# Performance work log

Measured on AMD Instinct MI355X. Metric: run time of the kernel, lower is better.

Reference implementation:

```python
import jax, jax.numpy as jnp
import numpy as np
import math

D_MODEL = 1024
NHEAD = 16
SEQ_LEN = 4096
K_PROJ = 16
HEAD_DIM = D_MODEL // NHEAD


def setup_inputs() -> dict:
    key = jax.random.key(0)
    ks = jax.random.split(key, 11)
    x = jax.random.normal(ks[0], (4, SEQ_LEN, D_MODEL), dtype=jnp.float32)
    s = 1.0 / math.sqrt(D_MODEL)
    Wq = jax.random.uniform(ks[1], (D_MODEL, D_MODEL), minval=-s, maxval=s)
    bq = jax.random.uniform(ks[2], (D_MODEL,), minval=-s, maxval=s)
    Wk = jax.random.uniform(ks[3], (D_MODEL, D_MODEL), minval=-s, maxval=s)
    bk = jax.random.uniform(ks[4], (D_MODEL,), minval=-s, maxval=s)
    Wv = jax.random.uniform(ks[5], (D_MODEL, D_MODEL), minval=-s, maxval=s)
    bv = jax.random.uniform(ks[6], (D_MODEL,), minval=-s, maxval=s)
    Wo = jax.random.uniform(ks[7], (D_MODEL, D_MODEL), minval=-s, maxval=s)
    bo = jax.random.uniform(ks[8], (D_MODEL,), minval=-s, maxval=s)
    E = jax.random.normal(ks[9], (NHEAD, K_PROJ, SEQ_LEN)) * 0.02
    F = jax.random.normal(ks[10], (NHEAD, K_PROJ, SEQ_LEN)) * 0.02
    return {"x": x, "Wq": Wq, "bq": bq, "Wk": Wk, "bk": bk,
            "Wv": Wv, "bv": bv, "Wo": Wo, "bo": bo, "E": E, "F": F}


def reference(x, Wq, bq, Wk, bk, Wv, bv, Wo, bo, E, F):
    B, N, D = x.shape
    # torch Linear: y = x @ W.T + b
    q = x @ Wq.T + bq
    k = x @ Wk.T + bk
    v = x @ Wv.T + bv
    # [B, H, N, Dh]
    def split_heads(t):
        return t.reshape(B, N, NHEAD, HEAD_DIM).transpose(0, 2, 1, 3)
    q, k, v = split_heads(q), split_heads(k), split_heads(v)
    # low-rank projections of K, V along sequence: [B, H, Kp, Dh]
    k_lin = jnp.einsum('bhnd,hkn->bhkd', k, E)
    v_lin = jnp.einsum('bhnd,hkn->bhkd', v, F)
    scores = jnp.einsum('bhnd,bhkd->bhnk', q, k_lin) / math.sqrt(HEAD_DIM)
    attn = jax.nn.softmax(scores, axis=-1)  # dropout is identity in eval
    out = jnp.einsum('bhnk,bhkd->bhnd', attn, v_lin)
    out = out.transpose(0, 2, 1, 3).reshape(B, N, D)
    return out @ Wo.T + bo
```

## Files before the change

kernel.cpp:

```cpp
#include <hip/hip_runtime.h>
#include <hip/hip_bf16.h>

#define SEQLEN 4096

typedef __bf16 bf16x8 __attribute__((ext_vector_type(8)));
typedef float f32x4 __attribute__((ext_vector_type(4)));
typedef __attribute__((ext_vector_type(8))) unsigned short u16x8;

__device__ inline float bf2f(unsigned short s) {
  union { unsigned u; float f; } t; t.u = ((unsigned)s) << 16; return t.f;
}
__device__ inline unsigned short f2bf(float f) {
  __hip_bfloat16 h = __float2bfloat16(f);
  return *reinterpret_cast<unsigned short*>(&h);
}

__device__ inline void gload_lds16(const void* g, void* l) {
  __builtin_amdgcn_global_load_lds(
      (const __attribute__((address_space(1))) unsigned int*)g,
      (__attribute__((address_space(3))) unsigned int*)l, 16, 0, 0);
}

__global__ void cvt_all(const float* __restrict__ x, const float* __restrict__ Wq,
                        const float* __restrict__ Wk, const float* __restrict__ Wv,
                        const float* __restrict__ Wo,
                        const float* __restrict__ bq, const float* __restrict__ bk,
                        const float* __restrict__ bv,
                        unsigned short* __restrict__ Xb,
                        unsigned short* __restrict__ Wqkv,
                        unsigned short* __restrict__ WoB, float* __restrict__ Bqkv) {
  long i = (long)blockIdx.x * 256 + threadIdx.x;
  const float* src;
  unsigned short* dst;
  long rel;
  if (i < 4194304) {
    src = x; dst = Xb; rel = i;
  } else if (i < 4456448) {
    src = Wq; dst = Wqkv; rel = i - 4194304;
  } else if (i < 4718592) {
    src = Wk; dst = Wqkv + 1048576; rel = i - 4456448;
  } else if (i < 4980736) {
    src = Wv; dst = Wqkv + 2097152; rel = i - 4718592;
  } else if (i < 5242880) {
    src = Wo; dst = WoB; rel = i - 4980736;
  } else if (i < 5243648) {
    long j = i - 5242880;
    const float* bsrc = (j < 256) ? bq : (j < 512) ? bk : bv;
    long jr = j & 255;
    reinterpret_cast<float4*>(Bqkv)[j] =
        reinterpret_cast<const float4*>(bsrc)[jr];
    return;
  } else {
    return;
  }
  float4 v = reinterpret_cast<const float4*>(src)[rel];
  ushort4 o;
  o.x = f2bf(v.x); o.y = f2bf(v.y); o.z = f2bf(v.z); o.w = f2bf(v.w);
  reinterpret_cast<ushort4*>(dst)[rel] = o;
}


#define MFMAQ(mh, nh, AR, BR)                                                   \
  __builtin_amdgcn_s_setprio(1);                                                \
  _Pragma("unroll")                                                             \
  for (int ks = 0; ks < 2; ++ks)                                                \
    _Pragma("unroll")                                                           \
    for (int mi = 0; mi < 4; ++mi)                                              \
      _Pragma("unroll")                                                         \
      for (int ni = 0; ni < 2; ++ni)                                            \
        acc[(mh) * 4 + mi][(nh) * 2 + ni] =                                     \
            __builtin_amdgcn_mfma_f32_16x16x32_bf16(                            \
                AR[mi][ks], BR[ni][ks], acc[(mh) * 4 + mi][(nh) * 2 + ni], 0, 0, 0); \
  __builtin_amdgcn_s_setprio(0);

#define LDA8(mi, sg) (*reinterpret_cast<const bf16x8*>(&as[((wr << 7) + (mi) * 16 + r16) * 64 + (sg) * 8]))
#define LDB8N(nh, ni, sg) (*reinterpret_cast<const bf16x8*>(&bs[(((nh) << 7) + (wc << 5) + (ni) * 16 + r16) * 64 + (sg) * 8]))

template <typename OUT_T>
__global__ __launch_bounds__(512, 2) void gemm8p(
    const unsigned short* __restrict__ A, const unsigned short* __restrict__ B,
    const float* __restrict__ bias, OUT_T* __restrict__ C, int M, int N, int K,
    int ldc) {
  extern __shared__ __align__(16) unsigned short lds[];

  const int tid = threadIdx.x;
  const int lane = tid & 63, wv = tid >> 6;
  const int wr = wv >> 2, wc = wv & 3;
  const int r16 = lane & 15, kg = lane >> 4;
  const int sg0 = (0 * 4 + kg) ^ (r16 & 7);
  const int sg1 = (1 * 4 + kg) ^ (r16 & 7);

  const int xcd = (int)blockIdx.x & 7;
  const int pos = (int)blockIdx.x >> 3;
  const int rpx = (M >> 8) >> 3;
  const int tile_m = xcd * rpx + (pos % rpx);
  const int tile_n = pos / rpx;
  const int brow = tile_m << 8, bcol = tile_n << 8;

  const unsigned short* Ag = A + (size_t)brow * K;
  const unsigned short* Bg = B + (size_t)bcol * K;

  const int sr = tid >> 3;
  const int sc = tid & 7;
  const int sgl = sc ^ (sr & 7);

  auto STG = [&](const unsigned short* G, unsigned short* dstbuf, int row0, int kt) {
    gload_lds16(G + (size_t)(row0 + sr) * K + (size_t)kt * 64 + sgl * 8,
                dstbuf + (row0 + sr) * 64 + sc * 8);
  };
  auto STGH = [&](int hw, int pb, int kt) {
    unsigned short* ab = lds + (pb << 14);
    unsigned short* bb = lds + 32768 + (pb << 14);
    if (hw == 0)      { STG(Ag, ab, 0, kt);   STG(Ag, ab, 128, kt); }
    else if (hw == 1) { STG(Bg, bb, 0, kt);   STG(Bg, bb, 64, kt); }
    else if (hw == 2) { STG(Bg, bb, 128, kt); STG(Bg, bb, 192, kt); }
    else              { STG(Ag, ab, 64, kt);  STG(Ag, ab, 192, kt); }
  };

  f32x4 acc[8][4];
#pragma unroll
  for (int m = 0; m < 8; ++m)
#pragma unroll
    for (int n = 0; n < 4; ++n) acc[m][n] = (f32x4)0.0f;

  const int NT = K >> 6;
  STGH(0, 0, 0); STGH(1, 0, 0); STGH(2, 0, 0); STGH(3, 0, 0);
  STGH(0, 1, 1); STGH(1, 1, 1); STGH(2, 1, 1);
  asm volatile("s_waitcnt vmcnt(6)" ::: "memory");
  __builtin_amdgcn_s_barrier();

  for (int t = 0; t < NT; ++t) {
    const int cur = t & 1;
    const unsigned short* as = lds + (cur << 14);
    const unsigned short* bs = lds + 32768 + (cur << 14);
    const int w1 = (t + 1 < NT) ? t + 1 : 0;
    const int w2 = (t + 2 < NT) ? t + 2 : t + 2 - NT;
    const int b1n = (t + 1) & 1;

    bf16x8 a[4][2], b0[2][2], b1[2][2];

    {
#pragma unroll
      for (int mi = 0; mi < 4; ++mi) { a[mi][0] = LDA8(mi, sg0); a[mi][1] = LDA8(mi, sg1); }
#pragma unroll
      for (int ni = 0; ni < 2; ++ni) { b0[ni][0] = LDB8N(0, ni, sg0); b0[ni][1] = LDB8N(0, ni, sg1); }
      STGH(3, b1n, w1);
      asm volatile("s_waitcnt lgkmcnt(8)" ::: "memory");
      __builtin_amdgcn_s_barrier();
      asm volatile("s_waitcnt lgkmcnt(0)" ::: "memory");
      MFMAQ(0, 0, a, b0);
      __builtin_amdgcn_s_barrier();
    }
    {
#pragma unroll
      for (int ni = 0; ni < 2; ++ni) { b1[ni][0] = LDB8N(1, ni, sg0); b1[ni][1] = LDB8N(1, ni, sg1); }
      STGH(0, cur, w2);
      __builtin_amdgcn_s_barrier();
      asm volatile("s_waitcnt lgkmcnt(0)" ::: "memory");
      MFMAQ(0, 1, a, b1);
      __builtin_amdgcn_s_barrier();
    }
    {
#pragma unroll
      for (int mi = 0; mi < 4; ++mi) { a[mi][0] = LDA8(4 + mi, sg0); a[mi][1] = LDA8(4 + mi, sg1); }
      STGH(1, cur, w2);
      __builtin_amdgcn_s_barrier();
      asm volatile("s_waitcnt lgkmcnt(0)" ::: "memory");
      MFMAQ(1, 1, a, b1);
      __builtin_amdgcn_s_barrier();
    }
    {
      STGH(2, cur, w2);
      MFMAQ(1, 0, a, b0);
      asm volatile("s_waitcnt vmcnt(6)" ::: "memory");
      __builtin_amdgcn_s_barrier();
    }
  }
  asm volatile("s_waitcnt vmcnt(0)" ::: "memory");

  if constexpr (sizeof(OUT_T) == 2) {
    __builtin_amdgcn_s_barrier();
    unsigned short* C2 = reinterpret_cast<unsigned short*>(C);
    float bvs[4];
#pragma unroll
    for (int n = 0; n < 4; ++n)
      bvs[n] = bias ? bias[bcol + ((n >> 1) << 7) + (wc << 5) + ((n & 1) << 4) + r16]
                    : 0.0f;
#pragma unroll
    for (int m = 0; m < 8; ++m) {
#pragma unroll
      for (int r = 0; r < 4; ++r) {
        int rw = m * 16 + kg * 4 + r;
        int xo = (rw & 12) << 2;
#pragma unroll
        for (int n = 0; n < 4; ++n) {
          lds[wv * 8192 + rw * 64 + ((n * 16 + r16) ^ xo)] =
              f2bf(acc[m][n][r] + bvs[n]);
        }
      }
    }
    __syncthreads();
#pragma unroll
    for (int p = 0; p < 16; ++p) {
      int grow = p * 16 + (tid >> 5);
      int g = tid & 31;
      int wvs = ((grow >> 7) << 2) + ((g >> 2) & 3);
      int row_l = grow & 127;
      int c4g = ((g >> 4) << 5) + ((g & 3) << 3);
      int src = wvs * 8192 + row_l * 64 + (c4g ^ ((row_l & 12) << 2));
      u16x8 vv = *reinterpret_cast<const u16x8*>(&lds[src]);
      *reinterpret_cast<u16x8*>(&C2[(size_t)(brow + grow) * ldc + bcol + g * 8]) = vv;
    }
  } else {
#pragma unroll
    for (int n = 0; n < 4; ++n) {
      int col = bcol + ((n >> 1) << 7) + (wc << 5) + ((n & 1) << 4) + r16;
      float bv = bias ? bias[col] : 0.0f;
#pragma unroll
      for (int m = 0; m < 8; ++m) {
#pragma unroll
        for (int r = 0; r < 4; ++r) {
          int row = brow + wr * 128 + m * 16 + kg * 4 + r;
          C[(size_t)row * ldc + col] = acc[m][n][r] + bv;
        }
      }
    }
  }
}

__global__ void kvlin_part(const unsigned short* __restrict__ qkv,
                           const float* __restrict__ E, const float* __restrict__ F,
                           float* __restrict__ part) {
  __shared__ __align__(16) unsigned short Ks[128 * 64], Vs[128 * 64];
  __shared__ __align__(16) float Es[16 * 128], Fs[16 * 128];
  const int tid = threadIdx.x;
  const int bid = blockIdx.x;
  const int bh = bid >> 3, ns = bid & 7;
  const int b = bh >> 4, h = bh & 15;
  const int d = tid & 63, kk = tid >> 6;
  float aK[4] = {0, 0, 0, 0}, aV[4] = {0, 0, 0, 0};
  for (int c = 0; c < 4; ++c) {
    int n0 = ns * 512 + c * 128;
#pragma unroll
    for (int it = 0; it < 4; ++it) {
      int f = it * 256 + tid;
      int row = f >> 3, ch = f & 7;
      const unsigned short* gk =
          qkv + (size_t)(b * SEQLEN + n0 + row) * 3072 + 1024 + h * 64 + ch * 8;
      gload_lds16(gk, &Ks[f * 8]);
      gload_lds16(gk + 1024, &Vs[f * 8]);
    }
#pragma unroll
    for (int it = 0; it < 2; ++it) {
      int f = it * 256 + tid;
      int k = f >> 5, ch = f & 31;
      const float* ge = E + (size_t)(h * 16 + k) * SEQLEN + n0 + ch * 4;
      const float* gf = F + (size_t)(h * 16 + k) * SEQLEN + n0 + ch * 4;
      gload_lds16(ge, &Es[f * 4]);
      gload_lds16(gf, &Fs[f * 4]);
    }
    __syncthreads();
    for (int n = 0; n < 128; ++n) {
      float kv = bf2f(Ks[n * 64 + d]);
      float vv = bf2f(Vs[n * 64 + d]);
#pragma unroll
      for (int j = 0; j < 4; ++j) {
        aK[j] += Es[(kk * 4 + j) * 128 + n] * kv;
        aV[j] += Fs[(kk * 4 + j) * 128 + n] * vv;
      }
    }
    __syncthreads();
  }
  size_t base = ((size_t)ns * 64 + bh) * 2048;
#pragma unroll
  for (int j = 0; j < 4; ++j) {
    part[base + (kk * 4 + j) * 64 + d] = aK[j];
    part[base + 1024 + (kk * 4 + j) * 64 + d] = aV[j];
  }
}

__global__ void kvlin_reduce(const float* __restrict__ part, float* __restrict__ out) {
  int i = blockIdx.x * 256 + threadIdx.x;
  float s = 0;
#pragma unroll
  for (int ns = 0; ns < 8; ++ns) s += part[(size_t)ns * 131072 + i];
  out[i] = s;
}

__global__ void attn_kernel(const unsigned short* __restrict__ qkv,
                            const float* __restrict__ kvlin,
                            unsigned short* __restrict__ aout) {
  __shared__ float kl[1024], vl[1024];
  const int tid = threadIdx.x;
  const int bid = blockIdx.x;
  const int bh = bid >> 4, nt = bid & 15;
  const int b = bh >> 4, h = bh & 15;
  for (int i = tid; i < 1024; i += 256) {
    kl[i] = kvlin[(size_t)bh * 2048 + i];
    vl[i] = kvlin[(size_t)bh * 2048 + 1024 + i];
  }
  __syncthreads();
  const int n = nt * 256 + tid;
  const unsigned short* qp = qkv + (size_t)(b * SEQLEN + n) * 3072 + h * 64;
  float q[64];
#pragma unroll
  for (int c2 = 0; c2 < 8; ++c2) {
    u16x8 v = *reinterpret_cast<const u16x8*>(qp + c2 * 8);
#pragma unroll
    for (int j = 0; j < 8; ++j) q[c2 * 8 + j] = bf2f(v[j]);
  }
  float s[16];
#pragma unroll
  for (int k = 0; k < 16; ++k) {
    float a = 0;
#pragma unroll
    for (int dd = 0; dd < 64; ++dd) a += q[dd] * kl[k * 64 + dd];
    s[k] = a * 0.125f;
  }
  float mx = s[0];
#pragma unroll
  for (int k = 1; k < 16; ++k) mx = fmaxf(mx, s[k]);
  float sum = 0;
#pragma unroll
  for (int k = 0; k < 16; ++k) { s[k] = __expf(s[k] - mx); sum += s[k]; }
  float inv = 1.0f / sum;
#pragma unroll
  for (int k = 0; k < 16; ++k) s[k] *= inv;
  unsigned short* op = aout + (size_t)(b * SEQLEN + n) * 1024 + h * 64;
#pragma unroll
  for (int d0 = 0; d0 < 8; ++d0) {
    float o[8] = {0, 0, 0, 0, 0, 0, 0, 0};
#pragma unroll
    for (int k = 0; k < 16; ++k) {
      float p = s[k];
#pragma unroll
      for (int j = 0; j < 8; ++j) o[j] += p * vl[k * 64 + d0 * 8 + j];
    }
    u16x8 pk;
#pragma unroll
    for (int j = 0; j < 8; ++j) pk[j] = f2bf(o[j]);
    *reinterpret_cast<u16x8*>(op + d0 * 8) = pk;
  }
}

extern "C" void kernel_launch(void* const* d_in, const int* in_sizes, int n_in,
                              void* d_out, int out_size, void* d_ws, size_t ws_size,
                              hipStream_t stream) {
  const float* x  = (const float*)d_in[0];
  const float* Wq = (const float*)d_in[1];
  const float* bq = (const float*)d_in[2];
  const float* Wk = (const float*)d_in[3];
  const float* bk = (const float*)d_in[4];
  const float* Wv = (const float*)d_in[5];
  const float* bv = (const float*)d_in[6];
  const float* Wo = (const float*)d_in[7];
  const float* bo = (const float*)d_in[8];
  const float* E  = (const float*)d_in[9];
  const float* F  = (const float*)d_in[10];
  float* out = (float*)d_out;

  char* ws = (char*)d_ws;
  unsigned short* Xb   = (unsigned short*)(ws);
  unsigned short* Wqkv = (unsigned short*)(ws + 33554432);
  unsigned short* WoB  = (unsigned short*)(ws + 39845888);
  float*          Bqkv = (float*)(ws + 41943040);
  unsigned short* QKV  = (unsigned short*)(ws + 41955328);
  float*          KVp  = (float*)(ws + 142618624);
  float*          KVl  = (float*)(ws + 146812928);
  unsigned short* AOut = Xb;

  (void)hipFuncSetAttribute(reinterpret_cast<const void*>(gemm8p<unsigned short>),
                            hipFuncAttributeMaxDynamicSharedMemorySize, 131072);
  (void)hipFuncSetAttribute(reinterpret_cast<const void*>(gemm8p<float>),
                            hipFuncAttributeMaxDynamicSharedMemorySize, 131072);

  cvt_all<<<20483, 256, 0, stream>>>(x, Wq, Wk, Wv, Wo, bq, bk, bv,
                                     Xb, Wqkv, WoB, Bqkv);

  gemm8p<unsigned short><<<768, 512, 131072, stream>>>(
      Xb, Wqkv, Bqkv, QKV, 16384, 3072, 1024, 3072);

  kvlin_part<<<512, 256, 0, stream>>>(QKV, E, F, KVp);
  kvlin_reduce<<<512, 256, 0, stream>>>(KVp, KVl);
  attn_kernel<<<1024, 256, 0, stream>>>(QKV, KVl, AOut);

  gemm8p<float><<<256, 512, 131072, stream>>>(
      AOut, WoB, bo, out, 16384, 1024, 1024, 1024);
}
```

Baseline: 261.3 us.

## Replace four-phase ping-pong GEMM main loop with simple double-buffered loop

Replaces the interleaved four-quadrant schedule, which split the global-to-LDS staging and the MFMA work across multiple barriers per K-tile, with a plain double-buffered loop. Each iteration now issues the whole next tile's loads up front, runs all 32 MFMAs per k-substep from LDS reads, then waits for all loads and takes one barrier. This cuts barrier count and scheduling complexity but gives up the finer-grained overlap of loads and compute. It also drops the extra barrier before the bf16 epilogue.

```diff
diff --git a/kernel.cpp b/kernel.cpp
--- a/kernel.cpp
+++ b/kernel.cpp
@@ -60,19 +60,6 @@
 }
 
 
-#define MFMAQ(mh, nh, AR, BR)                                                   \
-  __builtin_amdgcn_s_setprio(1);                                                \
-  _Pragma("unroll")                                                             \
-  for (int ks = 0; ks < 2; ++ks)                                                \
-    _Pragma("unroll")                                                           \
-    for (int mi = 0; mi < 4; ++mi)                                              \
-      _Pragma("unroll")                                                         \
-      for (int ni = 0; ni < 2; ++ni)                                            \
-        acc[(mh) * 4 + mi][(nh) * 2 + ni] =                                     \
-            __builtin_amdgcn_mfma_f32_16x16x32_bf16(                            \
-                AR[mi][ks], BR[ni][ks], acc[(mh) * 4 + mi][(nh) * 2 + ni], 0, 0, 0); \
-  __builtin_amdgcn_s_setprio(0);
-
 #define LDA8(mi, sg) (*reinterpret_cast<const bf16x8*>(&as[((wr << 7) + (mi) * 16 + r16) * 64 + (sg) * 8]))
 #define LDB8N(nh, ni, sg) (*reinterpret_cast<const bf16x8*>(&bs[(((nh) << 7) + (wc << 5) + (ni) * 16 + r16) * 64 + (sg) * 8]))
 
@@ -108,13 +95,13 @@
     gload_lds16(G + (size_t)(row0 + sr) * K + (size_t)kt * 64 + sgl * 8,
                 dstbuf + (row0 + sr) * 64 + sc * 8);
   };
-  auto STGH = [&](int hw, int pb, int kt) {
+  auto STGT = [&](int pb, int kt) {
     unsigned short* ab = lds + (pb << 14);
     unsigned short* bb = lds + 32768 + (pb << 14);
-    if (hw == 0)      { STG(Ag, ab, 0, kt);   STG(Ag, ab, 128, kt); }
-    else if (hw == 1) { STG(Bg, bb, 0, kt);   STG(Bg, bb, 64, kt); }
-    else if (hw == 2) { STG(Bg, bb, 128, kt); STG(Bg, bb, 192, kt); }
-    else              { STG(Ag, ab, 64, kt);  STG(Ag, ab, 192, kt); }
+    STG(Ag, ab, 0, kt);   STG(Ag, ab, 128, kt);
+    STG(Ag, ab, 64, kt);  STG(Ag, ab, 192, kt);
+    STG(Bg, bb, 0, kt);   STG(Bg, bb, 64, kt);
+    STG(Bg, bb, 128, kt); STG(Bg, bb, 192, kt);
   };
 
   f32x4 acc[8][4];
@@ -124,62 +111,38 @@
     for (int n = 0; n < 4; ++n) acc[m][n] = (f32x4)0.0f;
 
   const int NT = K >> 6;
-  STGH(0, 0, 0); STGH(1, 0, 0); STGH(2, 0, 0); STGH(3, 0, 0);
-  STGH(0, 1, 1); STGH(1, 1, 1); STGH(2, 1, 1);
-  asm volatile("s_waitcnt vmcnt(6)" ::: "memory");
+  STGT(0, 0);
+  asm volatile("s_waitcnt vmcnt(0)" ::: "memory");
   __builtin_amdgcn_s_barrier();
 
   for (int t = 0; t < NT; ++t) {
     const int cur = t & 1;
     const unsigned short* as = lds + (cur << 14);
     const unsigned short* bs = lds + 32768 + (cur << 14);
-    const int w1 = (t + 1 < NT) ? t + 1 : 0;
-    const int w2 = (t + 2 < NT) ? t + 2 : t + 2 - NT;
-    const int b1n = (t + 1) & 1;
-
-    bf16x8 a[4][2], b0[2][2], b1[2][2];
-
-    {
-#pragma unroll
-      for (int mi = 0; mi < 4; ++mi) { a[mi][0] = LDA8(mi, sg0); a[mi][1] = LDA8(mi, sg1); }
-#pragma unroll
-      for (int ni = 0; ni < 2; ++ni) { b0[ni][0] = LDB8N(0, ni, sg0); b0[ni][1] = LDB8N(0, ni, sg1); }
-      STGH(3, b1n, w1);
-      asm volatile("s_waitcnt lgkmcnt(8)" ::: "memory");
-      __builtin_amdgcn_s_barrier();
-      asm volatile("s_waitcnt lgkmcnt(0)" ::: "memory");
-      MFMAQ(0, 0, a, b0);
-      __builtin_amdgcn_s_barrier();
-    }
-    {
-#pragma unroll
-      for (int ni = 0; ni < 2; ++ni) { b1[ni][0] = LDB8N(1, ni, sg0); b1[ni][1] = LDB8N(1, ni, sg1); }
-      STGH(0, cur, w2);
-      __builtin_amdgcn_s_barrier();
-      asm volatile("s_waitcnt lgkmcnt(0)" ::: "memory");
-      MFMAQ(0, 1, a, b1);
-      __builtin_amdgcn_s_barrier();
-    }
-    {
-#pragma unroll
-      for (int mi = 0; mi < 4; ++mi) { a[mi][0] = LDA8(4 + mi, sg0); a[mi][1] = LDA8(4 + mi, sg1); }
-      STGH(1, cur, w2);
-      __builtin_amdgcn_s_barrier();
-      asm volatile("s_waitcnt lgkmcnt(0)" ::: "memory");
-      MFMAQ(1, 1, a, b1);
-      __builtin_amdgcn_s_barrier();
-    }
-    {
-      STGH(2, cur, w2);
-      MFMAQ(1, 0, a, b0);
-      asm volatile("s_waitcnt vmcnt(6)" ::: "memory");
-      __builtin_amdgcn_s_barrier();
-    }
-  }
-  asm volatile("s_waitcnt vmcnt(0)" ::: "memory");
+    if (t + 1 < NT) STGT(cur ^ 1, t + 1);
+
+    __builtin_amdgcn_s_setprio(1);
+#pragma unroll
+    for (int ks = 0; ks < 2; ++ks) {
+      const int sg = ks ? sg1 : sg0;
+      bf16x8 af[8], bfr[4];
+#pragma unroll
+      for (int mi = 0; mi < 8; ++mi) af[mi] = LDA8(mi, sg);
+#pragma unroll
+      for (int ni = 0; ni < 4; ++ni) bfr[ni] = LDB8N(ni >> 1, ni & 1, sg);
+#pragma unroll
+      for (int mi = 0; mi < 8; ++mi)
+#pragma unroll
+        for (int ni = 0; ni < 4; ++ni)
+          acc[mi][ni] = __builtin_amdgcn_mfma_f32_16x16x32_bf16(
+              af[mi], bfr[ni], acc[mi][ni], 0, 0, 0);
+    }
+    __builtin_amdgcn_s_setprio(0);
+    asm volatile("s_waitcnt vmcnt(0)" ::: "memory");
+    __builtin_amdgcn_s_barrier();
+  }
 
   if constexpr (sizeof(OUT_T) == 2) {
-    __builtin_amdgcn_s_barrier();
     unsigned short* C2 = reinterpret_cast<unsigned short*>(C);
     float bvs[4];
 #pragma unroll
```

New measurement: 254.7 us. 2.5% less time.
